# Optimization experiments

Measured on AMD Instinct MI355X. Metric: run time of the kernel, lower is better.

The kernel has to match this reference:

```python
import math
import jax, jax.numpy as jnp
import numpy as np

# ---- matryoshka config (matches init_kwargs) ----
NUM_HEADS = 16
KV_GROUPS = 4
KV_REPEATS = NUM_HEADS // KV_GROUPS
QK_SIZES = [32, 64, 128]      # output_sizes // num_heads
HEAD_SIZES = [32, 64, 128]
D_MODEL = 2048
NEG_INF = -1e9


def _heads_reorder_indices(num_heads, sizes, reverse=False):
    parts = [[] for _ in range(num_heads)]
    offset, prev = 0, 0
    for size in sizes:
        seg = size - prev
        for h in range(num_heads):
            parts[h].append(np.arange(offset, offset + seg))
            offset += seg
        prev = size
    reorder = np.concatenate([a for head in parts for a in head])
    if reverse:
        rev = np.empty_like(reorder)
        rev[reorder] = np.arange(len(reorder))
        reorder = rev
    return jnp.asarray(reorder, dtype=jnp.int32)

Q_REORDER = _heads_reorder_indices(NUM_HEADS, QK_SIZES)
K_REORDER = _heads_reorder_indices(KV_GROUPS, QK_SIZES)
V_REORDER = _heads_reorder_indices(KV_GROUPS, HEAD_SIZES)
O_REORDER = _heads_reorder_indices(NUM_HEADS, HEAD_SIZES, reverse=True)


def setup_inputs() -> dict:
    key = jax.random.key(0)
    ks = jax.random.split(key, 9)
    B, S = 2, 1024
    dq = NUM_HEADS * QK_SIZES[-1]      # 2048
    dkv_q = KV_GROUPS * QK_SIZES[-1]   # 512
    dkv_v = KV_GROUPS * HEAD_SIZES[-1] # 512
    dout = NUM_HEADS * HEAD_SIZES[-1]  # 2048
    s = 0.02
    return {
        "x": jax.random.normal(ks[0], (B, S, D_MODEL), jnp.float32),
        "mask": jnp.tril(jnp.ones((S, S), jnp.bool_)),
        "Wq": jax.random.normal(ks[1], (D_MODEL, dq), jnp.float32) * s,
        "bq": jnp.zeros((dq,), jnp.float32),
        "Wk": jax.random.normal(ks[2], (D_MODEL, dkv_q), jnp.float32) * s,
        "bk": jnp.zeros((dkv_q,), jnp.float32),
        "Wv": jax.random.normal(ks[3], (D_MODEL, dkv_v), jnp.float32) * s,
        "bv": jnp.zeros((dkv_v,), jnp.float32),
        "Wo": jax.random.normal(ks[4], (dout, D_MODEL), jnp.float32) * s,
        "bo": jnp.zeros((D_MODEL,), jnp.float32),
    }


def reference(x, mask, Wq, bq, Wk, bk, Wv, bv, Wo, bo):
    B, S, _ = x.shape
    H, G, R = NUM_HEADS, KV_GROUPS, KV_REPEATS
    Dq, Dh = QK_SIZES[-1], HEAD_SIZES[-1]

    # matryoshka projections (full-size forward) + buffer-indexed reorder
    q = (x @ Wq + bq)[..., Q_REORDER]
    k = (x @ Wk + bk)[..., K_REORDER]
    v = (x @ Wv + bv)[..., V_REORDER]

    q = q.reshape(B, S, H, Dq).transpose(0, 2, 1, 3)   # [B,H,S,Dq]
    k = k.reshape(B, S, G, Dq).transpose(0, 2, 1, 3)   # [B,G,S,Dq]
    v = v.reshape(B, S, G, Dh).transpose(0, 2, 1, 3)   # [B,G,S,Dh]

    # GQA expansion: each group repeated kv_repeats times consecutively
    k = jnp.repeat(k, R, axis=1)  # [B,H,S,Dq]
    v = jnp.repeat(v, R, axis=1)  # [B,H,S,Dh]

    add_mask = jnp.where(mask, 0.0, NEG_INF).astype(x.dtype)  # [S,S]

    xs = []
    dp_cum = 0.0
    prev_qk, prev_hd = 0, 0
    for qk, hd in zip(QK_SIZES, HEAD_SIZES):
        # dot product over the NEW qk segment, accumulated over prefixes
        dp = jnp.einsum('bhqd,bhkd->bhqk', q[..., prev_qk:qk], k[..., prev_qk:qk])
        dp_cum = dp_cum + dp
        logits = dp_cum * (1.0 / math.sqrt(qk)) + add_mask
        attn = jax.nn.softmax(logits, axis=-1)
        # output only the NEW value segment for this nesting level
        xs.append(jnp.einsum('bhqk,bhkd->bhqd', attn, v[..., prev_hd:hd]))
        prev_qk, prev_hd = qk, hd

    out = jnp.concatenate(xs, axis=-1)                 # [B,H,S,Dh]
    out = out.transpose(0, 2, 1, 3).reshape(B, S, H * Dh)
    out = out[..., O_REORDER]
    return out @ Wo + bo
```

## Files before the change

kernel.cpp:

```cpp
#include <hip/hip_runtime.h>

typedef __attribute__((ext_vector_type(8))) __bf16 bf16x8;
typedef __attribute__((ext_vector_type(8))) unsigned short u16x8;
typedef __attribute__((ext_vector_type(4))) float f32x4;

#define XBOFF 0
#define WQKVOFF (XBOFF + 2048 * 2048)
#define WOOFF   (WQKVOFF + 3072 * 2048)
#define QOFF    (WOOFF + 2048 * 2048)
#define KOFF    (QOFF + 2048 * 2048)
#define VTOFF   (KOFF + 2048 * 512)
#define AOFF    (VTOFF + 2048 * 512)
__device__ ushort g_scratch[AOFF + 2048 * 2048];

__device__ __forceinline__ int nest_map(int n, int H) {
    int h = n >> 7, j = n & 127;
    if (j < 32) return h * 32 + j;
    if (j < 64) return H * 32 + h * 32 + (j - 32);
    return H * 64 + h * 64 + (j - 64);
}

__device__ __forceinline__ ushort f2bf(float f) {
    unsigned u = __builtin_bit_cast(unsigned, f);
    u += 0x7fffu + ((u >> 16) & 1u);
    return (ushort)(u >> 16);
}
__device__ __forceinline__ bf16x8 ld_frag(const ushort* p) {
    return __builtin_bit_cast(bf16x8, *(const u16x8*)p);
}
__device__ __forceinline__ void glds16(const ushort* g, ushort* s) {
    __builtin_amdgcn_global_load_lds(
        (const __attribute__((address_space(1))) void*)g,
        (__attribute__((address_space(3))) void*)s, 16, 0, 0);
}

__global__ __launch_bounds__(256) void prep_kernel(
    const float* __restrict__ x,
    const float* __restrict__ Wq, const float* __restrict__ Wk,
    const float* __restrict__ Wv, const float* __restrict__ Wo)
{
    const int bx = blockIdx.x;
    const int tid = threadIdx.x;

    if (bx < 2048) {
        size_t i = ((size_t)bx * 256 + tid) * 8;
        float4 f0 = *(const float4*)&x[i];
        float4 f1 = *(const float4*)&x[i + 4];
        union { uint4 v; ushort u[8]; } a;
        a.u[0] = f2bf(f0.x); a.u[1] = f2bf(f0.y); a.u[2] = f2bf(f0.z); a.u[3] = f2bf(f0.w);
        a.u[4] = f2bf(f1.x); a.u[5] = f2bf(f1.y); a.u[6] = f2bf(f1.z); a.u[7] = f2bf(f1.w);
        *(uint4*)&g_scratch[XBOFF + i] = a.v;
        return;
    }

    const float* W; int rowlen, H, mode, dstoff, t;
    if (bx < 3072)      { W = Wq; rowlen = 2048; H = 16; mode = 0; dstoff = WQKVOFF;               t = bx - 2048; }
    else if (bx < 3328) { W = Wk; rowlen = 512;  H = 4;  mode = 0; dstoff = WQKVOFF + 2048 * 2048; t = bx - 3072; }
    else if (bx < 3584) { W = Wv; rowlen = 512;  H = 4;  mode = 0; dstoff = WQKVOFF + 2560 * 2048; t = bx - 3328; }
    else                { W = Wo; rowlen = 2048; H = 16; mode = 1; dstoff = WOOFF;                 t = bx - 3584; }
    const int k0 = (t & 31) * 64;
    const int n0 = (t >> 5) * 64;

    __shared__ ushort T[64][66];
    const int r = tid >> 3, oct = tid & 7;

    #pragma unroll
    for (int rep = 0; rep < 2; ++rep) {
        int rr = r + rep * 32;
        int wrow = mode ? nest_map(k0 + rr, 16) : (k0 + rr);
        int wcol = mode ? (n0 + oct * 8) : nest_map(n0 + oct * 8, H);
        float4 f0 = *(const float4*)&W[(size_t)wrow * rowlen + wcol];
        float4 f1 = *(const float4*)&W[(size_t)wrow * rowlen + wcol + 4];
        ushort* d = &T[rr][oct * 8];
        d[0] = f2bf(f0.x); d[1] = f2bf(f0.y); d[2] = f2bf(f0.z); d[3] = f2bf(f0.w);
        d[4] = f2bf(f1.x); d[5] = f2bf(f1.y); d[6] = f2bf(f1.z); d[7] = f2bf(f1.w);
    }
    __syncthreads();
    #pragma unroll
    for (int rep = 0; rep < 2; ++rep) {
        int rr = r + rep * 32;
        union { uint4 v; ushort u[8]; } cv;
        #pragma unroll
        for (int i = 0; i < 8; ++i) cv.u[i] = T[oct * 8 + i][rr];
        *(uint4*)&g_scratch[dstoff + (size_t)(n0 + rr) * 2048 + k0 + oct * 8] = cv.v;
    }
}

__global__ __launch_bounds__(256) void gemm128_kernel(
    const float* __restrict__ b0, const float* __restrict__ b1,
    const float* __restrict__ b2, float* __restrict__ oext, int mode)
{
    __shared__ __align__(16) ushort SH[2 * 128 * 64];
    ushort* As = SH;
    ushort* Bs = SH + 128 * 64;
    const int n0 = blockIdx.x * 128;
    const int m0 = blockIdx.y * 128;
    const int tid = threadIdx.x;
    const int lane = tid & 63, wid = tid >> 6;
    const int wm = wid & 1, wn = wid >> 1;
    const int quad = lane >> 4, l16 = lane & 15;

    const ushort* A  = g_scratch + (mode ? AOFF : XBOFF);
    const ushort* Bt = g_scratch + (mode ? WOOFF : WQKVOFF);

    const bool vpath = (mode == 0) && (n0 >= 2560);
    const float* bias; ushort* outS = nullptr; int c0, oldim, H;
    if (mode == 1)      { bias = b0; c0 = n0; oldim = 2048; H = 0; }
    else if (n0 < 2048) { bias = b0; outS = g_scratch + QOFF; c0 = n0;        oldim = 2048; H = 16; }
    else if (n0 < 2560) { bias = b1; outS = g_scratch + KOFF; c0 = n0 - 2048; oldim = 512;  H = 4; }
    else                { bias = b2; outS = nullptr;          c0 = n0 - 2560; oldim = 512;  H = 4; }

    const int lrow = lane >> 3;
    const int lchunk = (lane & 7) ^ (lrow & 7);

    f32x4 acc[4][4];
    #pragma unroll
    for (int a = 0; a < 4; ++a)
        #pragma unroll
        for (int c = 0; c < 4; ++c) acc[a][c] = f32x4{0.f, 0.f, 0.f, 0.f};

    for (int kt = 0; kt < 32; ++kt) {
        const int k0 = kt * 64;
        #pragma unroll
        for (int it = 0; it < 4; ++it) {
            int rb = it * 32 + wid * 8;
            int r  = rb + lrow;
            glds16(&A[(size_t)(m0 + r) * 2048 + k0 + lchunk * 8], &As[rb * 64]);
            glds16(&Bt[(size_t)(n0 + r) * 2048 + k0 + lchunk * 8], &Bs[rb * 64]);
        }
        __syncthreads();
        #pragma unroll
        for (int kc = 0; kc < 2; ++kc) {
            bf16x8 af[4], bf[4];
            #pragma unroll
            for (int s = 0; s < 4; ++s) {
                int ra = wm * 64 + s * 16 + l16;
                int rbv = wn * 64 + s * 16 + l16;
                int ch = kc * 4 + quad;
                af[s] = ld_frag(&As[ra * 64 + ((ch ^ (ra & 7)) * 8)]);
                bf[s] = ld_frag(&Bs[rbv * 64 + ((ch ^ (rbv & 7)) * 8)]);
            }
            #pragma unroll
            for (int sm = 0; sm < 4; ++sm)
                #pragma unroll
                for (int sn = 0; sn < 4; ++sn)
                    acc[sm][sn] = __builtin_amdgcn_mfma_f32_16x16x32_bf16(
                        af[sm], bf[sn], acc[sm][sn], 0, 0, 0);
        }
        __syncthreads();
    }

    if (vpath) {
        #pragma unroll
        for (int sm = 0; sm < 4; ++sm)
        #pragma unroll
        for (int sn = 0; sn < 4; ++sn)
        #pragma unroll
        for (int i = 0; i < 4; ++i) {
            int r = wm * 64 + sm * 16 + quad * 4 + i;
            int loc = wn * 64 + sn * 16 + l16;
            float v = acc[sm][sn][i] + bias[nest_map(c0 + loc, 4)];
            SH[loc * 128 + (r ^ ((loc & 7) << 3))] = f2bf(v);
        }
        __syncthreads();
        const int dloc = tid >> 1, half = tid & 1;
        const int gg = c0 >> 7, bb = m0 >> 10, sb = m0 & 1023;
        ushort* vt = g_scratch + VTOFF;
        #pragma unroll
        for (int j = 0; j < 8; ++j) {
            int r = half * 64 + j * 8;
            uint4 v = *(uint4*)&SH[dloc * 128 + (r ^ ((dloc & 7) << 3))];
            *(uint4*)&vt[((size_t)((bb * 4 + gg) * 128 + dloc)) * 1024 + sb + r] = v;
        }
    } else {
        #pragma unroll
        for (int sm = 0; sm < 4; ++sm)
        #pragma unroll
        for (int sn = 0; sn < 4; ++sn)
        #pragma unroll
        for (int i = 0; i < 4; ++i) {
            int row = m0 + wm * 64 + sm * 16 + quad * 4 + i;
            int loc = wn * 64 + sn * 16 + l16;
            float v = acc[sm][sn][i];
            if (mode == 1) {
                oext[(size_t)row * 2048 + c0 + loc] = v + bias[c0 + loc];
            } else {
                v += bias[nest_map(c0 + loc, H)];
                outS[(size_t)row * oldim + c0 + loc] = f2bf(v);
            }
        }
    }
}

__global__ __launch_bounds__(256) void attn_kernel()
{
    const ushort* qb = g_scratch + QOFF;
    const ushort* kb = g_scratch + KOFF;
    const ushort* vt = g_scratch + VTOFF;
    ushort* att = g_scratch + AOFF;

    __shared__ ushort Ks[64][136];
    __shared__ ushort Vt[128][72];
    __shared__ ushort Ps[64][72];

    const int x = blockIdx.x, h = blockIdx.y, b = blockIdx.z;
    const int ks_half = x >> 1;
    const int qt = ((x ^ b) & 1) ? ks_half : 15 - ks_half;
    const int g = h >> 2;
    const int q0 = qt * 64;
    const int tid = threadIdx.x;
    const int lane = tid & 63, w = tid >> 6;
    const int quad = lane >> 4, l16 = lane & 15;

    bf16x8 qa[4];
    {
        const ushort* qrow =
            qb + ((size_t)((b * 1024 + q0 + w * 16 + l16) * 16 + h)) * 128;
        #pragma unroll
        for (int kc = 0; kc < 4; ++kc)
            qa[kc] = ld_frag(qrow + kc * 32 + quad * 8);
    }

    float m_s[3][4], l_s[3][4];
    #pragma unroll
    for (int l = 0; l < 3; ++l)
        #pragma unroll
        for (int i = 0; i < 4; ++i) { m_s[l][i] = -1e9f; l_s[l][i] = 0.0f; }
    f32x4 oacc[8];
    #pragma unroll
    for (int t2 = 0; t2 < 8; ++t2) oacc[t2] = f32x4{0.f, 0.f, 0.f, 0.f};
    const f32x4 fz = {0.f, 0.f, 0.f, 0.f};

    for (int kt = 0; kt <= qt; ++kt) {
        const int k0 = kt * 64;
        {
            int r16 = tid >> 4, oct16 = tid & 15;
            #pragma unroll
            for (int rep = 0; rep < 4; ++rep) {
                int row = r16 + rep * 16;
                *(uint4*)&Ks[row][oct16 * 8] =
                    *(const uint4*)&kb[(size_t)((b * 1024 + k0 + row) * 4 + g) * 128 + oct16 * 8];
            }
            int oct = tid & 7, dr = tid >> 3;
            #pragma unroll
            for (int rep = 0; rep < 4; ++rep) {
                int d = dr + rep * 32;
                *(uint4*)&Vt[d][oct * 8] =
                    *(const uint4*)&vt[((size_t)((b * 4 + g) * 128 + d)) * 1024 + k0 + oct * 8];
            }
        }
        __syncthreads();

        const bool diag = (kt == qt);

        f32x4 s0[4], s1[4], s2[4];
        #pragma unroll
        for (int n = 0; n < 4; ++n)
            s0[n] = __builtin_amdgcn_mfma_f32_16x16x32_bf16(
                qa[0], ld_frag(&Ks[n * 16 + l16][quad * 8]), fz, 0, 0, 0);
        #pragma unroll
        for (int n = 0; n < 4; ++n)
            s1[n] = __builtin_amdgcn_mfma_f32_16x16x32_bf16(
                qa[1], ld_frag(&Ks[n * 16 + l16][32 + quad * 8]), s0[n], 0, 0, 0);
        #pragma unroll
        for (int n = 0; n < 4; ++n)
            s2[n] = __builtin_amdgcn_mfma_f32_16x16x32_bf16(
                qa[2], ld_frag(&Ks[n * 16 + l16][64 + quad * 8]), s1[n], 0, 0, 0);
        #pragma unroll
        for (int n = 0; n < 4; ++n)
            s2[n] = __builtin_amdgcn_mfma_f32_16x16x32_bf16(
                qa[3], ld_frag(&Ks[n * 16 + l16][96 + quad * 8]), s2[n], 0, 0, 0);

        float sv[3][4][4], mx[3][4];
        #pragma unroll
        for (int l = 0; l < 3; ++l)
            #pragma unroll
            for (int i = 0; i < 4; ++i) mx[l][i] = -1e9f;
        #pragma unroll
        for (int n = 0; n < 4; ++n)
            #pragma unroll
            for (int i = 0; i < 4; ++i) {
                bool msk = diag &&
                    (k0 + n * 16 + l16 > q0 + w * 16 + quad * 4 + i);
                float x0 = msk ? -1e9f : s0[n][i] * 0.1767766953f;
                float x1 = msk ? -1e9f : s1[n][i] * 0.125f;
                float x2 = msk ? -1e9f : s2[n][i] * 0.0883883476f;
                sv[0][n][i] = x0; mx[0][i] = fmaxf(mx[0][i], x0);
                sv[1][n][i] = x1; mx[1][i] = fmaxf(mx[1][i], x1);
                sv[2][n][i] = x2; mx[2][i] = fmaxf(mx[2][i], x2);
            }
        #pragma unroll
        for (int d = 1; d < 16; d <<= 1)
            #pragma unroll
            for (int l = 0; l < 3; ++l)
                #pragma unroll
                for (int i = 0; i < 4; ++i)
                    mx[l][i] = fmaxf(mx[l][i], __shfl_xor(mx[l][i], d, 64));
        float al[3][4], rs[3][4];
        #pragma unroll
        for (int l = 0; l < 3; ++l)
            #pragma unroll
            for (int i = 0; i < 4; ++i) {
                float mn = fmaxf(m_s[l][i], mx[l][i]);
                al[l][i] = __expf(m_s[l][i] - mn);
                m_s[l][i] = mn;
                rs[l][i] = 0.f;
            }
        #pragma unroll
        for (int n = 0; n < 4; ++n)
            #pragma unroll
            for (int l = 0; l < 3; ++l)
                #pragma unroll
                for (int i = 0; i < 4; ++i) {
                    float p = __expf(sv[l][n][i] - m_s[l][i]);
                    sv[l][n][i] = p;
                    rs[l][i] += p;
                }
        #pragma unroll
        for (int d = 1; d < 16; d <<= 1)
            #pragma unroll
            for (int l = 0; l < 3; ++l)
                #pragma unroll
                for (int i = 0; i < 4; ++i)
                    rs[l][i] += __shfl_xor(rs[l][i], d, 64);
        #pragma unroll
        for (int l = 0; l < 3; ++l)
            #pragma unroll
            for (int i = 0; i < 4; ++i)
                l_s[l][i] = l_s[l][i] * al[l][i] + rs[l][i];
        #pragma unroll
        for (int t = 0; t < 8; ++t) {
            int lvl = (t < 2) ? 0 : (t < 4) ? 1 : 2;
            #pragma unroll
            for (int i = 0; i < 4; ++i) oacc[t][i] *= al[lvl][i];
        }

        const int obase[3] = {0, 2, 4}, onts[3] = {2, 2, 4}, voffs[3] = {0, 32, 64};
        #pragma unroll
        for (int l = 0; l < 3; ++l) {
            #pragma unroll
            for (int n = 0; n < 4; ++n)
                #pragma unroll
                for (int i = 0; i < 4; ++i)
                    Ps[w * 16 + quad * 4 + i][n * 16 + l16] = f2bf(sv[l][n][i]);
            #pragma unroll
            for (int kc = 0; kc < 2; ++kc) {
                bf16x8 pa = ld_frag(&Ps[w * 16 + l16][kc * 32 + quad * 8]);
                #pragma unroll
                for (int t = 0; t < 4; ++t) {
                    if (t < onts[l]) {
                        int vd = voffs[l] + t * 16 + l16;
                        bf16x8 vf = ld_frag(&Vt[vd][kc * 32 + quad * 8]);
                        oacc[obase[l] + t] = __builtin_amdgcn_mfma_f32_16x16x32_bf16(
                            pa, vf, oacc[obase[l] + t], 0, 0, 0);
                    }
                }
            }
        }
        __syncthreads();
    }

    float inv[3][4];
    #pragma unroll
    for (int l = 0; l < 3; ++l)
        #pragma unroll
        for (int i = 0; i < 4; ++i) {
            float L = l_s[l][i];
            inv[l][i] = (L > 0.f) ? (1.0f / L) : 0.f;
        }
    #pragma unroll
    for (int t = 0; t < 8; ++t) {
        int lvl = (t < 2) ? 0 : (t < 4) ? 1 : 2;
        #pragma unroll
        for (int i = 0; i < 4; ++i) {
            int srow = q0 + w * 16 + quad * 4 + i;
            att[(size_t)((b * 1024 + srow) * 16 + h) * 128 + t * 16 + l16] =
                f2bf(oacc[t][i] * inv[lvl][i]);
        }
    }
}

extern "C" void kernel_launch(void* const* d_in, const int* in_sizes, int n_in,
                              void* d_out, int out_size, void* d_ws, size_t ws_size,
                              hipStream_t stream)
{
    const float* x  = (const float*)d_in[0];
    const float* Wq = (const float*)d_in[2];
    const float* bq = (const float*)d_in[3];
    const float* Wk = (const float*)d_in[4];
    const float* bk = (const float*)d_in[5];
    const float* Wv = (const float*)d_in[6];
    const float* bv = (const float*)d_in[7];
    const float* Wo = (const float*)d_in[8];
    const float* bo = (const float*)d_in[9];
    float* out = (float*)d_out;
    (void)d_ws; (void)ws_size;

    dim3 blk(256, 1, 1);
    hipLaunchKernelGGL(prep_kernel, dim3(4608), blk, 0, stream, x, Wq, Wk, Wv, Wo);
    hipLaunchKernelGGL(gemm128_kernel, dim3(24, 16), blk, 0, stream,
                       bq, bk, bv, (float*)nullptr, 0);
    hipLaunchKernelGGL(attn_kernel, dim3(16, 16, 2), blk, 0, stream);
    hipLaunchKernelGGL(gemm128_kernel, dim3(16, 16), blk, 0, stream,
                       bo, nullptr, nullptr, out, 1);
}
```

Baseline: 294.2 us.

## Shrink GEMM N-tile, add XCD-aware block remap, swizzle attention LDS, set priorities

```diff
diff --git a/kernel.cpp b/kernel.cpp
--- a/kernel.cpp
+++ b/kernel.cpp
@@ -11,7 +11,7 @@
 #define KOFF    (QOFF + 2048 * 2048)
 #define VTOFF   (KOFF + 2048 * 512)
 #define AOFF    (VTOFF + 2048 * 512)
-__device__ ushort g_scratch[AOFF + 2048 * 2048];
+__device__ __align__(16) ushort g_scratch[AOFF + 2048 * 2048];
 
 __device__ __forceinline__ int nest_map(int n, int H) {
     int h = n >> 7, j = n & 127;
@@ -90,11 +90,19 @@
     const float* __restrict__ b0, const float* __restrict__ b1,
     const float* __restrict__ b2, float* __restrict__ oext, int mode)
 {
-    __shared__ __align__(16) ushort SH[2 * 128 * 64];
+    __shared__ __align__(16) ushort SH[128 * 64 + 64 * 64];
     ushort* As = SH;
     ushort* Bs = SH + 128 * 64;
-    const int n0 = blockIdx.x * 128;
-    const int m0 = blockIdx.y * 128;
+
+    const int gx = gridDim.x;
+    const int nwg = gx * gridDim.y;
+    const int id = blockIdx.x + gx * blockIdx.y;
+    const int id2 = (id & 7) * (nwg >> 3) + (id >> 3);
+    const int m_idx = id2 / gx;
+    const int n_idx = id2 - m_idx * gx;
+    const int n0 = n_idx * 64;
+    const int m0 = m_idx * 128;
+
     const int tid = threadIdx.x;
     const int lane = tid & 63, wid = tid >> 6;
     const int wm = wid & 1, wn = wid >> 1;
@@ -113,11 +121,11 @@
     const int lrow = lane >> 3;
     const int lchunk = (lane & 7) ^ (lrow & 7);
 
-    f32x4 acc[4][4];
+    f32x4 acc[4][2];
     #pragma unroll
     for (int a = 0; a < 4; ++a)
         #pragma unroll
-        for (int c = 0; c < 4; ++c) acc[a][c] = f32x4{0.f, 0.f, 0.f, 0.f};
+        for (int c = 0; c < 2; ++c) acc[a][c] = f32x4{0.f, 0.f, 0.f, 0.f};
 
     for (int kt = 0; kt < 32; ++kt) {
         const int k0 = kt * 64;
@@ -126,24 +134,33 @@
             int rb = it * 32 + wid * 8;
             int r  = rb + lrow;
             glds16(&A[(size_t)(m0 + r) * 2048 + k0 + lchunk * 8], &As[rb * 64]);
+        }
+        #pragma unroll
+        for (int it = 0; it < 2; ++it) {
+            int rb = it * 32 + wid * 8;
+            int r  = rb + lrow;
             glds16(&Bt[(size_t)(n0 + r) * 2048 + k0 + lchunk * 8], &Bs[rb * 64]);
         }
         __syncthreads();
         #pragma unroll
         for (int kc = 0; kc < 2; ++kc) {
-            bf16x8 af[4], bf[4];
+            bf16x8 af[4], bf[2];
             #pragma unroll
             for (int s = 0; s < 4; ++s) {
                 int ra = wm * 64 + s * 16 + l16;
-                int rbv = wn * 64 + s * 16 + l16;
                 int ch = kc * 4 + quad;
                 af[s] = ld_frag(&As[ra * 64 + ((ch ^ (ra & 7)) * 8)]);
+            }
+            #pragma unroll
+            for (int s = 0; s < 2; ++s) {
+                int rbv = wn * 32 + s * 16 + l16;
+                int ch = kc * 4 + quad;
                 bf[s] = ld_frag(&Bs[rbv * 64 + ((ch ^ (rbv & 7)) * 8)]);
             }
             #pragma unroll
             for (int sm = 0; sm < 4; ++sm)
                 #pragma unroll
-                for (int sn = 0; sn < 4; ++sn)
+                for (int sn = 0; sn < 2; ++sn)
                     acc[sm][sn] = __builtin_amdgcn_mfma_f32_16x16x32_bf16(
                         af[sm], bf[sn], acc[sm][sn], 0, 0, 0);
         }
@@ -154,33 +171,35 @@
         #pragma unroll
         for (int sm = 0; sm < 4; ++sm)
         #pragma unroll
-        for (int sn = 0; sn < 4; ++sn)
+        for (int sn = 0; sn < 2; ++sn)
         #pragma unroll
         for (int i = 0; i < 4; ++i) {
             int r = wm * 64 + sm * 16 + quad * 4 + i;
-            int loc = wn * 64 + sn * 16 + l16;
+            int loc = wn * 32 + sn * 16 + l16;
             float v = acc[sm][sn][i] + bias[nest_map(c0 + loc, 4)];
             SH[loc * 128 + (r ^ ((loc & 7) << 3))] = f2bf(v);
         }
         __syncthreads();
-        const int dloc = tid >> 1, half = tid & 1;
-        const int gg = c0 >> 7, bb = m0 >> 10, sb = m0 & 1023;
+        const int dloc = tid >> 2;
+        const int qcol = (tid & 3) * 32;
+        const int gg = c0 >> 7, din = (c0 & 127);
+        const int bb = m0 >> 10, sb = m0 & 1023;
         ushort* vt = g_scratch + VTOFF;
         #pragma unroll
-        for (int j = 0; j < 8; ++j) {
-            int r = half * 64 + j * 8;
+        for (int j = 0; j < 4; ++j) {
+            int r = qcol + j * 8;
             uint4 v = *(uint4*)&SH[dloc * 128 + (r ^ ((dloc & 7) << 3))];
-            *(uint4*)&vt[((size_t)((bb * 4 + gg) * 128 + dloc)) * 1024 + sb + r] = v;
+            *(uint4*)&vt[((size_t)((bb * 4 + gg) * 128 + din + dloc)) * 1024 + sb + r] = v;
         }
     } else {
         #pragma unroll
         for (int sm = 0; sm < 4; ++sm)
         #pragma unroll
-        for (int sn = 0; sn < 4; ++sn)
+        for (int sn = 0; sn < 2; ++sn)
         #pragma unroll
         for (int i = 0; i < 4; ++i) {
             int row = m0 + wm * 64 + sm * 16 + quad * 4 + i;
-            int loc = wn * 64 + sn * 16 + l16;
+            int loc = wn * 32 + sn * 16 + l16;
             float v = acc[sm][sn][i];
             if (mode == 1) {
                 oext[(size_t)row * 2048 + c0 + loc] = v + bias[c0 + loc];
@@ -199,9 +218,9 @@
     const ushort* vt = g_scratch + VTOFF;
     ushort* att = g_scratch + AOFF;
 
-    __shared__ ushort Ks[64][136];
-    __shared__ ushort Vt[128][72];
-    __shared__ ushort Ps[64][72];
+    __shared__ __align__(16) ushort Ks[64 * 128];
+    __shared__ __align__(16) ushort Vt[128 * 64];
+    __shared__ __align__(16) ushort Ps[64 * 64];
 
     const int x = blockIdx.x, h = blockIdx.y, b = blockIdx.z;
     const int ks_half = x >> 1;
@@ -238,14 +257,14 @@
             #pragma unroll
             for (int rep = 0; rep < 4; ++rep) {
                 int row = r16 + rep * 16;
-                *(uint4*)&Ks[row][oct16 * 8] =
+                *(uint4*)&Ks[row * 128 + ((oct16 ^ (row & 7)) * 8)] =
                     *(const uint4*)&kb[(size_t)((b * 1024 + k0 + row) * 4 + g) * 128 + oct16 * 8];
             }
             int oct = tid & 7, dr = tid >> 3;
             #pragma unroll
             for (int rep = 0; rep < 4; ++rep) {
                 int d = dr + rep * 32;
-                *(uint4*)&Vt[d][oct * 8] =
+                *(uint4*)&Vt[d * 64 + ((oct ^ (d & 7)) * 8)] =
                     *(const uint4*)&vt[((size_t)((b * 4 + g) * 128 + d)) * 1024 + k0 + oct * 8];
             }
         }
@@ -254,22 +273,32 @@
         const bool diag = (kt == qt);
 
         f32x4 s0[4], s1[4], s2[4];
-        #pragma unroll
-        for (int n = 0; n < 4; ++n)
+        __builtin_amdgcn_s_setprio(1);
+        #pragma unroll
+        for (int n = 0; n < 4; ++n) {
+            int r = n * 16 + l16;
             s0[n] = __builtin_amdgcn_mfma_f32_16x16x32_bf16(
-                qa[0], ld_frag(&Ks[n * 16 + l16][quad * 8]), fz, 0, 0, 0);
-        #pragma unroll
-        for (int n = 0; n < 4; ++n)
+                qa[0], ld_frag(&Ks[r * 128 + (((0 + quad) ^ (r & 7)) * 8)]), fz, 0, 0, 0);
+        }
+        #pragma unroll
+        for (int n = 0; n < 4; ++n) {
+            int r = n * 16 + l16;
             s1[n] = __builtin_amdgcn_mfma_f32_16x16x32_bf16(
-                qa[1], ld_frag(&Ks[n * 16 + l16][32 + quad * 8]), s0[n], 0, 0, 0);
-        #pragma unroll
-        for (int n = 0; n < 4; ++n)
+                qa[1], ld_frag(&Ks[r * 128 + (((4 + quad) ^ (r & 7)) * 8)]), s0[n], 0, 0, 0);
+        }
+        #pragma unroll
+        for (int n = 0; n < 4; ++n) {
+            int r = n * 16 + l16;
             s2[n] = __builtin_amdgcn_mfma_f32_16x16x32_bf16(
-                qa[2], ld_frag(&Ks[n * 16 + l16][64 + quad * 8]), s1[n], 0, 0, 0);
-        #pragma unroll
-        for (int n = 0; n < 4; ++n)
+                qa[2], ld_frag(&Ks[r * 128 + (((8 + quad) ^ (r & 7)) * 8)]), s1[n], 0, 0, 0);
+        }
+        #pragma unroll
+        for (int n = 0; n < 4; ++n) {
+            int r = n * 16 + l16;
             s2[n] = __builtin_amdgcn_mfma_f32_16x16x32_bf16(
-                qa[3], ld_frag(&Ks[n * 16 + l16][96 + quad * 8]), s2[n], 0, 0, 0);
+                qa[3], ld_frag(&Ks[r * 128 + (((12 + quad) ^ (r & 7)) * 8)]), s2[n], 0, 0, 0);
+        }
+        __builtin_amdgcn_s_setprio(0);
 
         float sv[3][4][4], mx[3][4];
         #pragma unroll
@@ -341,21 +370,28 @@
             #pragma unroll
             for (int n = 0; n < 4; ++n)
                 #pragma unroll
-                for (int i = 0; i < 4; ++i)
-                    Ps[w * 16 + quad * 4 + i][n * 16 + l16] = f2bf(sv[l][n][i]);
+                for (int i = 0; i < 4; ++i) {
+                    int prow = w * 16 + quad * 4 + i;
+                    int col = n * 16 + l16;
+                    Ps[prow * 64 + ((((col >> 3) ^ (prow & 7)) << 3) | (col & 7))] =
+                        f2bf(sv[l][n][i]);
+                }
+            __builtin_amdgcn_s_setprio(1);
             #pragma unroll
             for (int kc = 0; kc < 2; ++kc) {
-                bf16x8 pa = ld_frag(&Ps[w * 16 + l16][kc * 32 + quad * 8]);
+                int prow = w * 16 + l16;
+                bf16x8 pa = ld_frag(&Ps[prow * 64 + (((kc * 4 + quad) ^ (prow & 7)) * 8)]);
                 #pragma unroll
                 for (int t = 0; t < 4; ++t) {
                     if (t < onts[l]) {
                         int vd = voffs[l] + t * 16 + l16;
-                        bf16x8 vf = ld_frag(&Vt[vd][kc * 32 + quad * 8]);
+                        bf16x8 vf = ld_frag(&Vt[vd * 64 + (((kc * 4 + quad) ^ (vd & 7)) * 8)]);
                         oacc[obase[l] + t] = __builtin_amdgcn_mfma_f32_16x16x32_bf16(
                             pa, vf, oacc[obase[l] + t], 0, 0, 0);
                     }
                 }
             }
+            __builtin_amdgcn_s_setprio(0);
         }
         __syncthreads();
     }
@@ -398,9 +434,9 @@
 
     dim3 blk(256, 1, 1);
     hipLaunchKernelGGL(prep_kernel, dim3(4608), blk, 0, stream, x, Wq, Wk, Wv, Wo);
-    hipLaunchKernelGGL(gemm128_kernel, dim3(24, 16), blk, 0, stream,
+    hipLaunchKernelGGL(gemm128_kernel, dim3(48, 16), blk, 0, stream,
                        bq, bk, bv, (float*)nullptr, 0);
     hipLaunchKernelGGL(attn_kernel, dim3(16, 16, 2), blk, 0, stream);
-    hipLaunchKernelGGL(gemm128_kernel, dim3(16, 16), blk, 0, stream,
+    hipLaunchKernelGGL(gemm128_kernel, dim3(32, 16), blk, 0, stream,
                        bo, nullptr, nullptr, out, 1);
 }
```

New measurement: 277.9 us. -5.5%, faster.
